# Kernel tuning notes

Hardware: AMD Instinct MI355X
Metric: run time of the kernel (lower is better)

The kernel has to match this reference:

```python
import jax, jax.numpy as jnp
import numpy as np
from jax import lax

B, T, C, H, W = 8, 2048, 128, 256, 16
LN_EPS = 1e-5


def setup_inputs() -> dict:
    key = jax.random.key(0)
    ks = jax.random.split(key, 8)
    s_ih = 1.0 / np.sqrt(H)
    return {
        "x": jax.random.normal(ks[0], (B, T, C), jnp.float32),
        "w_ih": jax.random.uniform(ks[1], (3 * H, C), jnp.float32, -s_ih, s_ih),
        "w_hh": jax.random.uniform(ks[2], (3 * H, H), jnp.float32, -s_ih, s_ih),
        "b_ih": jax.random.uniform(ks[3], (3 * H,), jnp.float32, -s_ih, s_ih),
        "b_hh": jax.random.uniform(ks[4], (3 * H,), jnp.float32, -s_ih, s_ih),
        "w_proj": jax.random.normal(ks[5], (H, H), jnp.float32) * (1.0 / np.sqrt(H)),
        "b_proj": jnp.zeros((H,), jnp.float32),
        "ln_gamma": jnp.ones((H,), jnp.float32),
        "ln_beta": jnp.zeros((H,), jnp.float32),
    }


def _sliding_gru(x, w_ih, w_hh, b_ih, b_hh):
    # x: [B,T,C]. Equivalent to running a GRU over each length-W left-padded
    # window ending at t, for all t, returning the final hidden state [B,T,H].
    pad = W - 1
    x_pad = jnp.pad(x, ((0, 0), (pad, 0), (0, 0)))  # [B, T+W-1, C]
    # Precompute input projection once (avoids the [B,T,W,C] unfold buffer).
    xi = jnp.einsum("btc,gc->btg", x_pad, w_ih) + b_ih  # [B, T+W-1, 3H]

    def step(h, w):
        # window step w sees x_pad[:, w : w+T, :] -> precomputed gates slice
        gi = lax.dynamic_slice_in_dim(xi, w, T, axis=1)  # [B,T,3H]
        gh = jnp.einsum("bth,gh->btg", h, w_hh) + b_hh   # [B,T,3H]
        gi_r, gi_z, gi_n = jnp.split(gi, 3, axis=-1)
        gh_r, gh_z, gh_n = jnp.split(gh, 3, axis=-1)
        r = jax.nn.sigmoid(gi_r + gh_r)
        z = jax.nn.sigmoid(gi_z + gh_z)
        n = jnp.tanh(gi_n + r * gh_n)
        h_new = (1.0 - z) * n + z * h
        return h_new, None

    h0 = jnp.zeros((B, T, H), x.dtype)
    h_final, _ = lax.scan(step, h0, jnp.arange(W))
    return h_final  # [B,T,H]


def reference(x, w_ih, w_hh, b_ih, b_hh, w_proj, b_proj, ln_gamma, ln_beta):
    feats = _sliding_gru(x, w_ih, w_hh, b_ih, b_hh)  # [B,T,H]
    y = jnp.einsum("bth,oh->bto", feats, w_proj) + b_proj
    mu = jnp.mean(y, axis=-1, keepdims=True)
    var = jnp.mean(jnp.square(y - mu), axis=-1, keepdims=True)
    y = (y - mu) * lax.rsqrt(var + LN_EPS) * ln_gamma + ln_beta
    return jax.nn.gelu(y, approximate=False)  # dropout is identity in eval
```

## Files before the change

### kernel.cpp

```cpp
#include <hip/hip_runtime.h>
#include <math.h>

typedef unsigned short u16;
typedef unsigned int   u32;
typedef __attribute__((ext_vector_type(8)))  short short8;
typedef __attribute__((ext_vector_type(16))) float f32x16;

#define NT 2048
#define NC 128
#define NH 256
#define NW 16
#define TPAD 2063

#define WS_GI_OFF 720896
#define WS_NEEDED (WS_GI_OFF + (size_t)8 * TPAD * 256 * 8)

__device__ __forceinline__ u16 f2bf(float f) {
  u32 u = __builtin_bit_cast(u32, f);
  u = u + 0x7fffu + ((u >> 16) & 1u);
  return (u16)(u >> 16);
}
__device__ __forceinline__ float bf2f(u16 v) {
  return __builtin_bit_cast(float, (u32)v << 16);
}
__device__ __forceinline__ float bflo(u32 w) {
  return __builtin_bit_cast(float, w << 16);
}
__device__ __forceinline__ float bfhi(u32 w) {
  return __builtin_bit_cast(float, w & 0xffff0000u);
}
__device__ __forceinline__ float nclamp(float v) {
  return fminf(fmaxf(v, -30.0f), 30.0f);
}
__device__ __forceinline__ float fsig(float x) {
  return __builtin_amdgcn_rcpf(1.0f + __builtin_amdgcn_exp2f(-1.44269504f * x));
}
__device__ __forceinline__ float ftanhf(float x) {
  float e = __builtin_amdgcn_exp2f(2.88539008f * x);
  return 1.0f - 2.0f * __builtin_amdgcn_rcpf(e + 1.0f);
}
__device__ __forceinline__ float gelu(float v) {
  return 0.5f * v * (1.0f + erff(v * 0.70710678118654752f));
}

__global__ void pack_w(const float* __restrict__ whh, const float* __restrict__ wih,
                       const float* __restrict__ wpr,
                       u16* __restrict__ whh_p, u16* __restrict__ wih_p,
                       u16* __restrict__ wpr_p) {
  int t = blockIdx.x * 256 + threadIdx.x;
  u16 v[8];
  if (t < 24576) {
    int lane = t & 63, kit = (t >> 6) & 15, nt = t >> 10;
    int wv = nt / 3, g = nt - wv * 3;
    int grow = g * 256 + wv * 32 + (lane & 31);
    int kb = kit * 16 + (lane >> 5) * 8;
    #pragma unroll
    for (int e = 0; e < 8; ++e) v[e] = f2bf(whh[grow * 256 + kb + e]);
    u32* d = (u32*)(whh_p + (size_t)t * 8);
    #pragma unroll
    for (int e = 0; e < 4; ++e) d[e] = (u32)v[2*e] | ((u32)v[2*e+1] << 16);
  } else if (t < 36864) {
    int t2 = t - 24576;
    int lane = t2 & 63, kit = (t2 >> 6) & 7, nt = t2 >> 9;
    int wv = nt / 3, g = nt - wv * 3;
    int grow = g * 256 + wv * 32 + (lane & 31);
    int kb = kit * 16 + (lane >> 5) * 8;
    #pragma unroll
    for (int e = 0; e < 8; ++e) v[e] = f2bf(wih[grow * 128 + kb + e]);
    u32* d = (u32*)(wih_p + (size_t)t2 * 8);
    #pragma unroll
    for (int e = 0; e < 4; ++e) d[e] = (u32)v[2*e] | ((u32)v[2*e+1] << 16);
  } else if (t < 45056) {
    int t3 = t - 36864;
    int lane = t3 & 63, kit = (t3 >> 6) & 15, nt = t3 >> 10;
    int o = nt * 32 + (lane & 31);
    int kb = kit * 16 + (lane >> 5) * 8;
    #pragma unroll
    for (int e = 0; e < 8; ++e) v[e] = f2bf(wpr[o * 256 + kb + e]);
    u32* d = (u32*)(wpr_p + (size_t)t3 * 8);
    #pragma unroll
    for (int e = 0; e < 4; ++e) d[e] = (u32)v[2*e] | ((u32)v[2*e+1] << 16);
  }
}

__global__ __launch_bounds__(512, 2) void xi_kernel(
    const float* __restrict__ x, const float* __restrict__ b_ih,
    const u16* __restrict__ wih_p, uint2* __restrict__ gi) {
  __shared__ u16 xs[64 * 128];
  const int tid = threadIdx.x, wv = tid >> 6, lane = tid & 63;
  const int ml = lane & 31, lh = lane >> 5;
  const int b = blockIdx.x / 33, chunk = blockIdx.x % 33;
  const int tp0 = chunk * 64;
  const int j = wv * 32 + ml;

  {
    int r = tid >> 3, c0e = (tid & 7) * 16;
    int xr = tp0 + r - (NW - 1);
    float vv[16];
    if (xr >= 0 && xr < NT) {
      const float4* src = (const float4*)(x + ((long)b * NT + xr) * NC + c0e);
      #pragma unroll
      for (int q = 0; q < 4; ++q) {
        float4 f = src[q];
        vv[q*4+0] = f.x; vv[q*4+1] = f.y; vv[q*4+2] = f.z; vv[q*4+3] = f.w;
      }
    } else {
      #pragma unroll
      for (int q = 0; q < 16; ++q) vv[q] = 0.0f;
    }
    int byb = r * 256 + c0e * 2;
    int sw = (r & 15) << 4;
    #pragma unroll
    for (int ch = 0; ch < 2; ++ch) {
      u32 q0 = (u32)f2bf(vv[ch*8+0]) | ((u32)f2bf(vv[ch*8+1]) << 16);
      u32 q1 = (u32)f2bf(vv[ch*8+2]) | ((u32)f2bf(vv[ch*8+3]) << 16);
      u32 q2 = (u32)f2bf(vv[ch*8+4]) | ((u32)f2bf(vv[ch*8+5]) << 16);
      u32 q3 = (u32)f2bf(vv[ch*8+6]) | ((u32)f2bf(vv[ch*8+7]) << 16);
      *(uint4*)((char*)xs + ((byb + ch * 16) ^ sw)) = make_uint4(q0, q1, q2, q3);
    }
  }
  __syncthreads();

  const float bi0 = b_ih[j], bi1 = b_ih[NH + j], bi2 = b_ih[2 * NH + j];
  f32x16 acc[2][3];
  #pragma unroll
  for (int mt = 0; mt < 2; ++mt) {
    #pragma unroll
    for (int e = 0; e < 16; ++e) {
      acc[mt][0][e] = bi0; acc[mt][1][e] = bi1; acc[mt][2][e] = bi2;
    }
  }

  const int sw0 = (ml & 15) << 4;
  #pragma unroll 4
  for (int kit = 0; kit < 8; ++kit) {
    short8 a0 = *(const short8*)((const char*)xs +
                  ((ml * 256 + kit * 32 + lh * 16) ^ sw0));
    short8 a1 = *(const short8*)((const char*)xs +
                  (((ml + 32) * 256 + kit * 32 + lh * 16) ^ sw0));
    #pragma unroll
    for (int g = 0; g < 3; ++g) {
      short8 bfr = __builtin_bit_cast(short8,
                     ((const uint4*)wih_p)[((wv * 3 + g) * 8 + kit) * 64 + lane]);
      acc[0][g] = __builtin_amdgcn_mfma_f32_32x32x16_bf16(a0, bfr, acc[0][g], 0, 0, 0);
      acc[1][g] = __builtin_amdgcn_mfma_f32_32x32x16_bf16(a1, bfr, acc[1][g], 0, 0, 0);
    }
  }

  #pragma unroll
  for (int mt = 0; mt < 2; ++mt) {
    #pragma unroll
    for (int rg = 0; rg < 16; ++rg) {
      int m = mt * 32 + (rg & 3) + 8 * (rg >> 2) + 4 * lh;
      int tp = tp0 + m;
      if (tp < TPAD) {
        u32 rz = (u32)f2bf(acc[mt][0][rg]) | ((u32)f2bf(acc[mt][1][rg]) << 16);
        u32 nn = (u32)f2bf(acc[mt][2][rg]);
        gi[((long)b * TPAD + tp) * 256 + j] = make_uint2(rz, nn);
      }
    }
  }
}

__global__ __launch_bounds__(1024, 4) void gru_main(
    const float* __restrict__ b_hh,
    const u16* __restrict__ whh_p, const u16* __restrict__ wpr_p,
    const uint2* __restrict__ gi,
    const float* __restrict__ c256_0, const float* __restrict__ c256_1,
    const float* __restrict__ c256_2, float* __restrict__ out) {
  __shared__ u32 rz_lds[79 * 256];
  __shared__ u16 n_lds[79 * 256];
  __shared__ u16 hbuf[64 * 256];
  const int tid = threadIdx.x, wv4 = tid >> 6, lane = tid & 63;
  const int ml = lane & 31, lh = lane >> 5;
  const int mt = wv4 >> 3, wvg = wv4 & 7;
  const int wg = (blockIdx.x & 7) * 32 + (blockIdx.x >> 3);
  const int bidx = wg >> 5, t0 = (wg & 31) * 64;
  const long R0 = (long)wg * 64;
  const int j = wvg * 32 + ml;
  const int arow = mt * 32 + ml;

  const float *gp, *bpp, *bep;
  {
    float v0 = c256_0[0], v1 = c256_1[0];
    if (fabsf(v0 - 1.0f) < 0.25f)      { gp = c256_0; bpp = c256_1; bep = c256_2; }
    else if (fabsf(v1 - 1.0f) < 0.25f) { gp = c256_1; bpp = c256_0; bep = c256_2; }
    else                               { gp = c256_2; bpp = c256_0; bep = c256_1; }
  }

  const float bhr = b_hh[j], bhz = b_hh[NH + j], bnh = b_hh[2 * NH + j];

  {
    const uint2* gwin = gi + ((long)bidx * TPAD + t0) * 256;
    for (int idx = tid; idx < 79 * 256; idx += 1024) {
      uint2 v = gwin[idx];
      rz_lds[idx] = v.x;
      n_lds[idx] = (u16)v.y;
    }
  }
  __syncthreads();

  float hreg[16];
  #pragma unroll
  for (int rg = 0; rg < 16; ++rg) hreg[rg] = 0.0f;

  const int swh = (ml & 15) << 4;

  for (int s = 0; s < NW; ++s) {
    f32x16 acc[3];
    #pragma unroll
    for (int e = 0; e < 16; ++e) {
      acc[0][e] = bhr; acc[1][e] = bhz; acc[2][e] = bnh;
    }

    if (s > 0) {
      #pragma unroll 4
      for (int kit = 0; kit < 16; ++kit) {
        short8 a0 = *(const short8*)((const char*)hbuf +
                      ((arow * 512 + kit * 32 + lh * 16) ^ swh));
        #pragma unroll
        for (int g = 0; g < 3; ++g) {
          short8 bfr = __builtin_bit_cast(short8,
                         ((const uint4*)whh_p)[(((wvg * 3 + g) * 16) + kit) * 64 + lane]);
          acc[g] = __builtin_amdgcn_mfma_f32_32x32x16_bf16(a0, bfr, acc[g], 0, 0, 0);
        }
      }
    }
    __syncthreads();

    #pragma unroll
    for (int rg = 0; rg < 16; ++rg) {
      int m = mt * 32 + (rg & 3) + 8 * (rg >> 2) + 4 * lh;
      int ro = (s + m) * 256 + j;
      u32 rzv = rz_lds[ro];
      float gnv = bf2f(n_lds[ro]);
      float r = fsig(bflo(rzv) + acc[0][rg]);
      float z = fsig(bfhi(rzv) + acc[1][rg]);
      float n = ftanhf(gnv + r * acc[2][rg]);
      float hv = n + z * (hreg[rg] - n);
      hreg[rg] = hv;
      *(u16*)((char*)hbuf + ((m * 512 + j * 2) ^ ((m & 15) << 4))) = f2bf(hv);
    }
    __syncthreads();
  }

  f32x16 pc;
  #pragma unroll
  for (int e = 0; e < 16; ++e) pc[e] = 0.0f;
  #pragma unroll 4
  for (int kit = 0; kit < 16; ++kit) {
    short8 a0 = *(const short8*)((const char*)hbuf +
                  ((arow * 512 + kit * 32 + lh * 16) ^ swh));
    short8 bfr = __builtin_bit_cast(short8,
                   ((const uint4*)wpr_p)[(wvg * 16 + kit) * 64 + lane]);
    pc = __builtin_amdgcn_mfma_f32_32x32x16_bf16(a0, bfr, pc, 0, 0, 0);
  }
  const float bp = bpp[j];
  __syncthreads();
  #pragma unroll
  for (int rg = 0; rg < 16; ++rg) {
    int m = mt * 32 + (rg & 3) + 8 * (rg >> 2) + 4 * lh;
    *(u16*)((char*)hbuf + ((m * 512 + j * 2) ^ ((m & 15) << 4))) = f2bf(pc[rg] + bp);
  }
  __syncthreads();

  {
    int m = tid >> 4, cg = (tid & 15) * 16;
    int sw = (m & 15) << 4;
    float v[16];
    #pragma unroll
    for (int q = 0; q < 2; ++q) {
      uint4 raw = *(const uint4*)((char*)hbuf + ((m * 512 + cg * 2 + q * 16) ^ sw));
      u32 w4[4] = {raw.x, raw.y, raw.z, raw.w};
      #pragma unroll
      for (int e = 0; e < 4; ++e) {
        v[q * 8 + e * 2]     = bflo(w4[e]);
        v[q * 8 + e * 2 + 1] = bfhi(w4[e]);
      }
    }
    float s1 = 0.0f, s2 = 0.0f;
    #pragma unroll
    for (int i = 0; i < 16; ++i) { s1 += v[i]; s2 += v[i] * v[i]; }
    #pragma unroll
    for (int d = 1; d < 16; d <<= 1) {
      s1 += __shfl_xor(s1, d, 64);
      s2 += __shfl_xor(s2, d, 64);
    }
    float mu = s1 * (1.0f / 256.0f);
    float var = s2 * (1.0f / 256.0f) - mu * mu;
    if (!(var > 0.0f)) var = 0.0f;
    float rstd = rsqrtf(var + 1e-5f);
    float* od = out + (R0 + m) * NH + cg;
    #pragma unroll
    for (int q = 0; q < 4; ++q) {
      int i0 = q * 4;
      float o0 = gelu((v[i0]     - mu) * rstd * gp[cg + i0]     + bep[cg + i0]);
      float o1 = gelu((v[i0 + 1] - mu) * rstd * gp[cg + i0 + 1] + bep[cg + i0 + 1]);
      float o2 = gelu((v[i0 + 2] - mu) * rstd * gp[cg + i0 + 2] + bep[cg + i0 + 2]);
      float o3 = gelu((v[i0 + 3] - mu) * rstd * gp[cg + i0 + 3] + bep[cg + i0 + 3]);
      *(float4*)(od + i0) = make_float4(o0, o1, o2, o3);
    }
  }
}

__device__ __forceinline__ short8 cvt8(const float* p) {
  float4 a = *(const float4*)p, b = *(const float4*)(p + 4);
  u16 v0 = f2bf(a.x), v1 = f2bf(a.y), v2 = f2bf(a.z), v3 = f2bf(a.w);
  u16 v4 = f2bf(b.x), v5 = f2bf(b.y), v6 = f2bf(b.z), v7 = f2bf(b.w);
  u32 r0 = (u32)v0 | ((u32)v1 << 16), r1 = (u32)v2 | ((u32)v3 << 16);
  u32 r2 = (u32)v4 | ((u32)v5 << 16), r3 = (u32)v6 | ((u32)v7 << 16);
  uint4 r = make_uint4(r0, r1, r2, r3);
  return __builtin_bit_cast(short8, r);
}

__global__ __launch_bounds__(512, 2) void gru_fb(
    const float* __restrict__ x, const float* __restrict__ b_ih, const float* __restrict__ b_hh,
    const float* __restrict__ wih, const float* __restrict__ whh, const float* __restrict__ wpr,
    const float* __restrict__ c256_0, const float* __restrict__ c256_1,
    const float* __restrict__ c256_2, float* __restrict__ out) {
  __shared__ u16 xs[80 * 128];
  __shared__ u16 hb[2][64 * 256];
  const int tid = threadIdx.x, wv = tid >> 6, lane = tid & 63;
  const int ml = lane & 31, lh = lane >> 5;
  const int wg = blockIdx.x;
  const int bidx = wg >> 5, t0 = (wg & 31) * 64;
  const long R0 = (long)wg * 64;
  const int j = wv * 32 + ml;
  const float *gp, *bpp, *bep;
  {
    float v0 = c256_0[0], v1 = c256_1[0];
    if (fabsf(v0 - 1.0f) < 0.25f)      { gp = c256_0; bpp = c256_1; bep = c256_2; }
    else if (fabsf(v1 - 1.0f) < 0.25f) { gp = c256_1; bpp = c256_0; bep = c256_2; }
    else                               { gp = c256_2; bpp = c256_0; bep = c256_1; }
  }
  const float br  = b_ih[j] + b_hh[j];
  const float bz  = b_ih[NH + j] + b_hh[NH + j];
  const float bni = b_ih[2 * NH + j];
  const float bnh = b_hh[2 * NH + j];
  {
    int r = tid >> 3, c0e = (tid & 7) * 16;
    #pragma unroll
    for (int pass = 0; pass < 2; ++pass) {
      int rr = r + pass * 64;
      if (rr < 79) {
        int tx = t0 + rr - (NW - 1);
        float vv[16];
        if (tx >= 0) {
          const float4* src = (const float4*)(x + ((long)bidx * NT + tx) * NC + c0e);
          #pragma unroll
          for (int q = 0; q < 4; ++q) {
            float4 f = src[q];
            vv[q*4+0] = f.x; vv[q*4+1] = f.y; vv[q*4+2] = f.z; vv[q*4+3] = f.w;
          }
        } else {
          #pragma unroll
          for (int q = 0; q < 16; ++q) vv[q] = 0.0f;
        }
        int byb = rr * 256 + c0e * 2;
        int sw = (rr & 15) << 4;
        #pragma unroll
        for (int ch = 0; ch < 2; ++ch) {
          u32 q0 = (u32)f2bf(vv[ch*8+0]) | ((u32)f2bf(vv[ch*8+1]) << 16);
          u32 q1 = (u32)f2bf(vv[ch*8+2]) | ((u32)f2bf(vv[ch*8+3]) << 16);
          u32 q2 = (u32)f2bf(vv[ch*8+4]) | ((u32)f2bf(vv[ch*8+5]) << 16);
          u32 q3 = (u32)f2bf(vv[ch*8+6]) | ((u32)f2bf(vv[ch*8+7]) << 16);
          *(uint4*)((char*)xs + ((byb + ch * 16) ^ sw)) = make_uint4(q0, q1, q2, q3);
        }
      }
    }
  }
  __syncthreads();
  float hreg[2][16];
  #pragma unroll
  for (int mt = 0; mt < 2; ++mt)
    #pragma unroll
    for (int rg = 0; rg < 16; ++rg) hreg[mt][rg] = 0.0f;
  const int swh = (ml & 15) << 4;
  for (int s = 0; s < NW; ++s) {
    f32x16 acc[2][4];
    #pragma unroll
    for (int mt = 0; mt < 2; ++mt)
      #pragma unroll
      for (int g = 0; g < 4; ++g)
        #pragma unroll
        for (int e = 0; e < 16; ++e) acc[mt][g][e] = 0.0f;
    if (s > 0) {
      const u16* hc = hb[(s + 1) & 1];
      #pragma unroll 4
      for (int kit = 0; kit < 16; ++kit) {
        short8 a0 = *(const short8*)((const char*)hc +
                      ((ml * 512 + kit * 32 + lh * 16) ^ swh));
        short8 a1 = *(const short8*)((const char*)hc +
                      (((ml + 32) * 512 + kit * 32 + lh * 16) ^ swh));
        #pragma unroll
        for (int g = 0; g < 3; ++g) {
          short8 bfr = cvt8(whh + (g * 256 + wv * 32 + ml) * 256 + kit * 16 + lh * 8);
          const int ga = (g == 2) ? 3 : g;
          acc[0][ga] = __builtin_amdgcn_mfma_f32_32x32x16_bf16(a0, bfr, acc[0][ga], 0, 0, 0);
          acc[1][ga] = __builtin_amdgcn_mfma_f32_32x32x16_bf16(a1, bfr, acc[1][ga], 0, 0, 0);
        }
      }
    }
    {
      int r0 = s + ml;
      int sw0 = (r0 & 15) << 4;
      #pragma unroll 4
      for (int kit = 0; kit < 8; ++kit) {
        short8 a0 = *(const short8*)((const char*)xs +
                      ((r0 * 256 + kit * 32 + lh * 16) ^ sw0));
        short8 a1 = *(const short8*)((const char*)xs +
                      (((r0 + 32) * 256 + kit * 32 + lh * 16) ^ sw0));
        #pragma unroll
        for (int g = 0; g < 3; ++g) {
          short8 bfr = cvt8(wih + (g * 256 + wv * 32 + ml) * 128 + kit * 16 + lh * 8);
          acc[0][g] = __builtin_amdgcn_mfma_f32_32x32x16_bf16(a0, bfr, acc[0][g], 0, 0, 0);
          acc[1][g] = __builtin_amdgcn_mfma_f32_32x32x16_bf16(a1, bfr, acc[1][g], 0, 0, 0);
        }
      }
    }
    u16* hn = hb[s & 1];
    #pragma unroll
    for (int mt = 0; mt < 2; ++mt) {
      #pragma unroll
      for (int rg = 0; rg < 16; ++rg) {
        int m = mt * 32 + (rg & 3) + 8 * (rg >> 2) + 4 * lh;
        float r = fsig(nclamp(acc[mt][0][rg] + br));
        float z = fsig(nclamp(acc[mt][1][rg] + bz));
        float n = ftanhf(nclamp(acc[mt][2][rg] + bni + r * (acc[mt][3][rg] + bnh)));
        float hv = n + z * (hreg[mt][rg] - n);
        hreg[mt][rg] = hv;
        *(u16*)((char*)hn + ((m * 512 + j * 2) ^ ((m & 15) << 4))) = f2bf(hv);
      }
    }
    __syncthreads();
  }
  f32x16 pc[2];
  #pragma unroll
  for (int mt = 0; mt < 2; ++mt)
    #pragma unroll
    for (int e = 0; e < 16; ++e) pc[mt][e] = 0.0f;
  const u16* hf = hb[1];
  #pragma unroll 4
  for (int kit = 0; kit < 16; ++kit) {
    short8 a0 = *(const short8*)((const char*)hf +
                  ((ml * 512 + kit * 32 + lh * 16) ^ swh));
    short8 a1 = *(const short8*)((const char*)hf +
                  (((ml + 32) * 512 + kit * 32 + lh * 16) ^ swh));
    short8 bfr = cvt8(wpr + (wv * 32 + ml) * 256 + kit * 16 + lh * 8);
    pc[0] = __builtin_amdgcn_mfma_f32_32x32x16_bf16(a0, bfr, pc[0], 0, 0, 0);
    pc[1] = __builtin_amdgcn_mfma_f32_32x32x16_bf16(a1, bfr, pc[1], 0, 0, 0);
  }
  const float bp = bpp[j];
  #pragma unroll
  for (int mt = 0; mt < 2; ++mt) {
    #pragma unroll
    for (int rg = 0; rg < 16; ++rg) {
      int m = mt * 32 + (rg & 3) + 8 * (rg >> 2) + 4 * lh;
      *(u16*)((char*)hb[0] + ((m * 512 + j * 2) ^ ((m & 15) << 4))) = f2bf(pc[mt][rg] + bp);
    }
  }
  __syncthreads();
  {
    int m = tid >> 3, cg = (tid & 7) * 32;
    int sw = (m & 15) << 4;
    float v[32];
    #pragma unroll
    for (int q = 0; q < 4; ++q) {
      uint4 raw = *(const uint4*)((char*)hb[0] + ((m * 512 + cg * 2 + q * 16) ^ sw));
      u32 w4[4] = {raw.x, raw.y, raw.z, raw.w};
      #pragma unroll
      for (int e = 0; e < 4; ++e) {
        v[q * 8 + e * 2]     = bflo(w4[e]);
        v[q * 8 + e * 2 + 1] = bfhi(w4[e]);
      }
    }
    float s1 = 0.0f, s2 = 0.0f;
    #pragma unroll
    for (int i = 0; i < 32; ++i) { s1 += v[i]; s2 += v[i] * v[i]; }
    #pragma unroll
    for (int d = 1; d < 8; d <<= 1) {
      s1 += __shfl_xor(s1, d, 64);
      s2 += __shfl_xor(s2, d, 64);
    }
    float mu = s1 * (1.0f / 256.0f);
    float var = s2 * (1.0f / 256.0f) - mu * mu;
    if (!(var > 0.0f)) var = 0.0f;
    float rstd = rsqrtf(var + 1e-5f);
    float* od = out + (R0 + m) * NH + cg;
    #pragma unroll
    for (int q = 0; q < 8; ++q) {
      int i0 = q * 4;
      float o0 = gelu((v[i0]     - mu) * rstd * gp[cg + i0]     + bep[cg + i0]);
      float o1 = gelu((v[i0 + 1] - mu) * rstd * gp[cg + i0 + 1] + bep[cg + i0 + 1]);
      float o2 = gelu((v[i0 + 2] - mu) * rstd * gp[cg + i0 + 2] + bep[cg + i0 + 2]);
      float o3 = gelu((v[i0 + 3] - mu) * rstd * gp[cg + i0 + 3] + bep[cg + i0 + 3]);
      *(float4*)(od + i0) = make_float4(o0, o1, o2, o3);
    }
  }
}

extern "C" void kernel_launch(void* const* d_in, const int* in_sizes, int n_in,
                              void* d_out, int out_size, void* d_ws, size_t ws_size,
                              hipStream_t stream) {
  (void)out_size;
  const float *x = nullptr, *wih = nullptr, *whh = nullptr, *b768a = nullptr,
              *b768b = nullptr, *wpr = nullptr, *c0 = nullptr, *c1 = nullptr,
              *c2 = nullptr;
  int n768 = 0, n256 = 0;
  for (int i = 0; i < n_in; ++i) {
    const float* p = (const float*)d_in[i];
    switch (in_sizes[i]) {
      case 2097152: x = p; break;
      case 98304:   wih = p; break;
      case 196608:  whh = p; break;
      case 65536:   wpr = p; break;
      case 768:     { if (n768 == 0) b768a = p; else b768b = p; ++n768; } break;
      case 256:     { if (n256 == 0) c0 = p; else if (n256 == 1) c1 = p; else c2 = p; ++n256; } break;
      default: break;
    }
  }
  char* ws = (char*)d_ws;
  u16* whh_p = (u16*)(ws + 0);
  u16* wih_p = (u16*)(ws + 393216);
  u16* wpr_p = (u16*)(ws + 589824);
  uint2* gi  = (uint2*)(ws + WS_GI_OFF);
  float* outp = (float*)d_out;

  if (ws_size >= WS_NEEDED) {
    pack_w<<<dim3(176), dim3(256), 0, stream>>>(whh, wih, wpr, whh_p, wih_p, wpr_p);
    xi_kernel<<<dim3(264), dim3(512), 0, stream>>>(x, b768a, wih_p, gi);
    gru_main<<<dim3(256), dim3(1024), 0, stream>>>(b768b, whh_p, wpr_p, gi,
                                                   c0, c1, c2, outp);
  } else {
    gru_fb<<<dim3(256), dim3(512), 0, stream>>>(x, b768a, b768b, wih, whh, wpr,
                                                c0, c1, c2, outp);
  }
}
```

Measured before the change: 210.4 us.

## Transpose GRU MFMA operands for vectorized gate reads and fold r/z biases

Swaps the A/B operands of the recurrent and projection MFMAs so each lane's accumulator holds consecutive hidden units for a single time row. The gate-input LDS buffers are stored with an XOR swizzle, which allows vectorized uint4/uint2 gate loads and packed 8-byte h writes instead of scalar 16-bit accesses. The r and z hidden biases are folded into the precomputed input projection, and the n-gate bias stays in per-lane registers. The aim is fewer LDS instructions and less per-step bias work in the serial 16-step loop. The trade-off is extra registers for the bias arrays and the risk of new LDS bank conflicts from the changed access pattern.

Result: no change. 210.1 us (-0.2%).

```diff
diff --git a/kernel.cpp b/kernel.cpp
--- a/kernel.cpp
+++ b/kernel.cpp
@@ -85,6 +85,7 @@
 
 __global__ __launch_bounds__(512, 2) void xi_kernel(
     const float* __restrict__ x, const float* __restrict__ b_ih,
+    const float* __restrict__ b_hh,
     const u16* __restrict__ wih_p, uint2* __restrict__ gi) {
   __shared__ u16 xs[64 * 128];
   const int tid = threadIdx.x, wv = tid >> 6, lane = tid & 63;
@@ -121,7 +122,9 @@
   }
   __syncthreads();
 
-  const float bi0 = b_ih[j], bi1 = b_ih[NH + j], bi2 = b_ih[2 * NH + j];
+  const float bi0 = b_ih[j] + b_hh[j];
+  const float bi1 = b_ih[NH + j] + b_hh[NH + j];
+  const float bi2 = b_ih[2 * NH + j];
   f32x16 acc[2][3];
   #pragma unroll
   for (int mt = 0; mt < 2; ++mt) {
@@ -177,8 +180,8 @@
   const int wg = (blockIdx.x & 7) * 32 + (blockIdx.x >> 3);
   const int bidx = wg >> 5, t0 = (wg & 31) * 64;
   const long R0 = (long)wg * 64;
-  const int j = wvg * 32 + ml;
-  const int arow = mt * 32 + ml;
+  const int m = mt * 32 + ml;
+  const int jb = wvg * 32;
 
   const float *gp, *bpp, *bep;
   {
@@ -188,14 +191,21 @@
     else                               { gp = c256_2; bpp = c256_0; bep = c256_1; }
   }
 
-  const float bhr = b_hh[j], bhz = b_hh[NH + j], bnh = b_hh[2 * NH + j];
+  float bnh_r[16];
+  #pragma unroll
+  for (int q = 0; q < 4; ++q) {
+    float4 bq = *(const float4*)(b_hh + 2 * NH + jb + q * 8 + 4 * lh);
+    bnh_r[q*4+0] = bq.x; bnh_r[q*4+1] = bq.y; bnh_r[q*4+2] = bq.z; bnh_r[q*4+3] = bq.w;
+  }
 
   {
     const uint2* gwin = gi + ((long)bidx * TPAD + t0) * 256;
     for (int idx = tid; idx < 79 * 256; idx += 1024) {
       uint2 v = gwin[idx];
-      rz_lds[idx] = v.x;
-      n_lds[idx] = (u16)v.y;
+      int row = idx >> 8, jj = idx & 255;
+      int jx = row * 256 + (jj ^ ((row & 15) << 2));
+      rz_lds[jx] = v.x;
+      n_lds[jx] = (u16)v.y;
     }
   }
   __syncthreads();
@@ -209,37 +219,52 @@
   for (int s = 0; s < NW; ++s) {
     f32x16 acc[3];
     #pragma unroll
-    for (int e = 0; e < 16; ++e) {
-      acc[0][e] = bhr; acc[1][e] = bhz; acc[2][e] = bnh;
-    }
+    for (int g = 0; g < 3; ++g)
+      #pragma unroll
+      for (int e = 0; e < 16; ++e) acc[g][e] = 0.0f;
 
     if (s > 0) {
       #pragma unroll 4
       for (int kit = 0; kit < 16; ++kit) {
-        short8 a0 = *(const short8*)((const char*)hbuf +
-                      ((arow * 512 + kit * 32 + lh * 16) ^ swh));
+        short8 hfr = *(const short8*)((const char*)hbuf +
+                       ((m * 512 + kit * 32 + lh * 16) ^ swh));
         #pragma unroll
         for (int g = 0; g < 3; ++g) {
-          short8 bfr = __builtin_bit_cast(short8,
+          short8 wfr = __builtin_bit_cast(short8,
                          ((const uint4*)whh_p)[(((wvg * 3 + g) * 16) + kit) * 64 + lane]);
-          acc[g] = __builtin_amdgcn_mfma_f32_32x32x16_bf16(a0, bfr, acc[g], 0, 0, 0);
+          acc[g] = __builtin_amdgcn_mfma_f32_32x32x16_bf16(wfr, hfr, acc[g], 0, 0, 0);
         }
       }
     }
     __syncthreads();
 
-    #pragma unroll
-    for (int rg = 0; rg < 16; ++rg) {
-      int m = mt * 32 + (rg & 3) + 8 * (rg >> 2) + 4 * lh;
-      int ro = (s + m) * 256 + j;
-      u32 rzv = rz_lds[ro];
-      float gnv = bf2f(n_lds[ro]);
-      float r = fsig(bflo(rzv) + acc[0][rg]);
-      float z = fsig(bfhi(rzv) + acc[1][rg]);
-      float n = ftanhf(gnv + r * acc[2][rg]);
-      float hv = n + z * (hreg[rg] - n);
-      hreg[rg] = hv;
-      *(u16*)((char*)hbuf + ((m * 512 + j * 2) ^ ((m & 15) << 4))) = f2bf(hv);
+    {
+      int row = s + m;
+      int swj = (row & 15) << 2;
+      int rbase = row * 256;
+      #pragma unroll
+      for (int q = 0; q < 4; ++q) {
+        int j0 = jb + q * 8 + 4 * lh;
+        int jx = rbase + (j0 ^ swj);
+        uint4 rzq = *(const uint4*)(rz_lds + jx);
+        uint2 nq  = *(const uint2*)(n_lds + jx);
+        u32 rza[4] = {rzq.x, rzq.y, rzq.z, rzq.w};
+        float na[4] = {bflo(nq.x), bfhi(nq.x), bflo(nq.y), bfhi(nq.y)};
+        u16 hw[4];
+        #pragma unroll
+        for (int e = 0; e < 4; ++e) {
+          int rg = q * 4 + e;
+          float r = fsig(bflo(rza[e]) + acc[0][rg]);
+          float z = fsig(bfhi(rza[e]) + acc[1][rg]);
+          float n = ftanhf(na[e] + r * (acc[2][rg] + bnh_r[rg]));
+          float hv = n + z * (hreg[rg] - n);
+          hreg[rg] = hv;
+          hw[e] = f2bf(hv);
+        }
+        u32 w0 = (u32)hw[0] | ((u32)hw[1] << 16);
+        u32 w1 = (u32)hw[2] | ((u32)hw[3] << 16);
+        *(uint2*)((char*)hbuf + ((m * 512 + j0 * 2) ^ swh)) = make_uint2(w0, w1);
+      }
     }
     __syncthreads();
   }
@@ -249,28 +274,35 @@
   for (int e = 0; e < 16; ++e) pc[e] = 0.0f;
   #pragma unroll 4
   for (int kit = 0; kit < 16; ++kit) {
-    short8 a0 = *(const short8*)((const char*)hbuf +
-                  ((arow * 512 + kit * 32 + lh * 16) ^ swh));
-    short8 bfr = __builtin_bit_cast(short8,
+    short8 hfr = *(const short8*)((const char*)hbuf +
+                   ((m * 512 + kit * 32 + lh * 16) ^ swh));
+    short8 wfr = __builtin_bit_cast(short8,
                    ((const uint4*)wpr_p)[(wvg * 16 + kit) * 64 + lane]);
-    pc = __builtin_amdgcn_mfma_f32_32x32x16_bf16(a0, bfr, pc, 0, 0, 0);
-  }
-  const float bp = bpp[j];
+    pc = __builtin_amdgcn_mfma_f32_32x32x16_bf16(wfr, hfr, pc, 0, 0, 0);
+  }
   __syncthreads();
   #pragma unroll
-  for (int rg = 0; rg < 16; ++rg) {
-    int m = mt * 32 + (rg & 3) + 8 * (rg >> 2) + 4 * lh;
-    *(u16*)((char*)hbuf + ((m * 512 + j * 2) ^ ((m & 15) << 4))) = f2bf(pc[rg] + bp);
+  for (int q = 0; q < 4; ++q) {
+    int o0 = jb + q * 8 + 4 * lh;
+    float4 bq = *(const float4*)(bpp + o0);
+    u16 yw[4];
+    yw[0] = f2bf(pc[q*4+0] + bq.x);
+    yw[1] = f2bf(pc[q*4+1] + bq.y);
+    yw[2] = f2bf(pc[q*4+2] + bq.z);
+    yw[3] = f2bf(pc[q*4+3] + bq.w);
+    u32 w0 = (u32)yw[0] | ((u32)yw[1] << 16);
+    u32 w1 = (u32)yw[2] | ((u32)yw[3] << 16);
+    *(uint2*)((char*)hbuf + ((m * 512 + o0 * 2) ^ swh)) = make_uint2(w0, w1);
   }
   __syncthreads();
 
   {
-    int m = tid >> 4, cg = (tid & 15) * 16;
-    int sw = (m & 15) << 4;
+    int mr = tid >> 4, cg = (tid & 15) * 16;
+    int sw = (mr & 15) << 4;
     float v[16];
     #pragma unroll
     for (int q = 0; q < 2; ++q) {
-      uint4 raw = *(const uint4*)((char*)hbuf + ((m * 512 + cg * 2 + q * 16) ^ sw));
+      uint4 raw = *(const uint4*)((char*)hbuf + ((mr * 512 + cg * 2 + q * 16) ^ sw));
       u32 w4[4] = {raw.x, raw.y, raw.z, raw.w};
       #pragma unroll
       for (int e = 0; e < 4; ++e) {
@@ -290,7 +322,7 @@
     float var = s2 * (1.0f / 256.0f) - mu * mu;
     if (!(var > 0.0f)) var = 0.0f;
     float rstd = rsqrtf(var + 1e-5f);
-    float* od = out + (R0 + m) * NH + cg;
+    float* od = out + (R0 + mr) * NH + cg;
     #pragma unroll
     for (int q = 0; q < 4; ++q) {
       int i0 = q * 4;
@@ -528,7 +560,7 @@
 
   if (ws_size >= WS_NEEDED) {
     pack_w<<<dim3(176), dim3(256), 0, stream>>>(whh, wih, wpr, whh_p, wih_p, wpr_p);
-    xi_kernel<<<dim3(264), dim3(512), 0, stream>>>(x, b768a, wih_p, gi);
+    xi_kernel<<<dim3(264), dim3(512), 0, stream>>>(x, b768a, b768b, wih_p, gi);
     gru_main<<<dim3(256), dim3(1024), 0, stream>>>(b768b, whh_p, wpr_p, gi,
                                                    c0, c1, c2, outp);
   } else {
```
